# Kernel tuning notes

Hardware: AMD Instinct MI355X
Metric: run time of the kernel (lower is better)

## Reference

```python
import jax, jax.numpy as jnp
import numpy as np

N, M, D = 131072, 8, 128
TAU = 1.0
E_CONST = float(np.e)


def setup_inputs() -> dict:
    key = jax.random.key(0)
    ks = jax.random.split(key, 6)
    x = jax.random.normal(ks[0], (N, M, D), dtype=jnp.float32)
    q = jax.random.uniform(ks[1], (N, M), dtype=jnp.float32)  # per-mode energies
    w = 0.1 * jax.random.uniform(ks[2], (M,), dtype=jnp.float32)
    b = 0.1 * jax.random.uniform(ks[3], (M,), dtype=jnp.float32)
    gammas = jax.random.uniform(ks[4], (M, M), dtype=jnp.float32)  # in (0,1)
    G = 0.1 * jax.random.normal(ks[5], (M,), dtype=jnp.float32)
    bias = jnp.zeros((M,), dtype=jnp.float32)
    qmin = jnp.zeros((M,), dtype=jnp.float32)
    return {"x": x, "q": q, "w": w, "b": b, "gammas": gammas,
            "G": G, "bias": bias, "qmin": qmin}


def reference(x, q, w, b, gammas, G, bias, qmin):
    e = jnp.float32(E_CONST)
    # correction (eval mode): shift by running min, clamp at e so phi > 0
    corr = jnp.maximum(q - qmin[None, :] + e, e)          # [N, M]
    phi = (1.0 + w)[None, :] * corr + b[None, :]          # [N, M]
    # symmetrized gamma: g[i,j] = gammas[min(i,j), max(i,j)]
    idx = jnp.arange(gammas.shape[0])
    g_sym = jnp.where(idx[:, None] < idx[None, :], gammas, gammas.T)  # [M, M]
    # pairwise power-weighted partial energies: phi_i^g * phi_j^(1-g)
    partials = phi[:, :, None] ** g_sym[None] * phi[:, None, :] ** (1.0 - g_sym)[None]  # [N, M, M]
    modal = jnp.sum(partials, axis=-1)                    # [N, M]
    logs = jax.nn.log_softmax(-TAU * modal, axis=-1)
    alphas = jnp.exp(logs)                                # [N, M]
    # gated attention over modes
    betas = jax.nn.relu(jnp.tanh(G[None, :] * alphas + bias[None, :]))  # [N, M]
    return betas[:, :, None] * x                          # [N, M, D]
```

## Files before the change

kernel.cpp:

```cpp
#include <hip/hip_runtime.h>
#include <math.h>

#define NROWS 131072
#define M 8
#define D 128
#define RPB 32
#define E_CONST 2.71828182845904523536f

__global__ __launch_bounds__(256) void emma_fused2(
    const float* __restrict__ x, const float* __restrict__ q,
    const float* __restrict__ w, const float* __restrict__ b,
    const float* __restrict__ gammas, const float* __restrict__ G,
    const float* __restrict__ bias, const float* __restrict__ qmin,
    float* __restrict__ out)
{
    __shared__ float s_beta[RPB][M];

    const int tid = threadIdx.x;
    const int r   = tid >> 3;
    const int i   = tid & 7;
    const int n   = blockIdx.x * RPB + r;

    {
        const float4 q0 = *reinterpret_cast<const float4*>(q + (size_t)n * M);
        const float4 q1 = *reinterpret_cast<const float4*>(q + (size_t)n * M + 4);
        float qv[M] = {q0.x, q0.y, q0.z, q0.w, q1.x, q1.y, q1.z, q1.w};

        float lphi[M];
        #pragma unroll
        for (int m = 0; m < M; ++m) {
            float corr = fmaxf(qv[m] - qmin[m] + E_CONST, E_CONST);
            float phi  = fmaf(w[m], corr, corr) + b[m];
            lphi[m] = logf(phi);
        }

        float myl = lphi[0];
        #pragma unroll
        for (int m = 1; m < M; ++m) if (i == m) myl = lphi[m];

        float s = 0.0f;
        #pragma unroll
        for (int j = 0; j < M; ++j) {
            int lo = (i < j) ? i : j;
            int hi = (i < j) ? j : i;
            float g = gammas[lo * M + hi];
            s += expf(fmaf(g, myl - lphi[j], lphi[j]));
        }

        float neg = -s;
        float mx = neg;
        #pragma unroll
        for (int d = 1; d < 8; d <<= 1) mx = fmaxf(mx, __shfl_xor(mx, d, 8));
        float e = expf(neg - mx);
        float sum = e;
        #pragma unroll
        for (int d = 1; d < 8; d <<= 1) sum += __shfl_xor(sum, d, 8);
        float alpha = e / sum;

        float t = tanhf(fmaf(G[i], alpha, bias[i]));
        s_beta[r][i] = fmaxf(t, 0.0f);
    }
    __syncthreads();

    const size_t base = (size_t)blockIdx.x * (RPB * M * D);
    const float4* __restrict__ x4 = reinterpret_cast<const float4*>(x + base);
    float4* __restrict__ o4       = reinterpret_cast<float4*>(out + base);
    const int mm = tid >> 5;

    #pragma unroll 4
    for (int rr = 0; rr < RPB; ++rr) {
        const float beta = s_beta[rr][mm];
        float4 v = x4[(size_t)rr * 256 + tid];
        v.x *= beta; v.y *= beta; v.z *= beta; v.w *= beta;
        o4[(size_t)rr * 256 + tid] = v;
    }
}

extern "C" void kernel_launch(void* const* d_in, const int* in_sizes, int n_in,
                              void* d_out, int out_size, void* d_ws, size_t ws_size,
                              hipStream_t stream) {
    const float* x      = (const float*)d_in[0];
    const float* q      = (const float*)d_in[1];
    const float* w      = (const float*)d_in[2];
    const float* b      = (const float*)d_in[3];
    const float* gammas = (const float*)d_in[4];
    const float* G      = (const float*)d_in[5];
    const float* bias   = (const float*)d_in[6];
    const float* qmin   = (const float*)d_in[7];
    float* out = (float*)d_out;

    emma_fused2<<<NROWS / RPB, 256, 0, stream>>>(
        x, q, w, b, gammas, G, bias, qmin, out);
}
```

Measured before the change: 214.6 us.

## Skip x loads for zero-gated modes and use nontemporal batched streaming

Reworks the scaling phase so each wave handles units of 32 lanes of float4 for a given row and mode. When every lane in the wave sees beta equal to zero, it writes zeros without reading x at all, which cuts read traffic for modes the ReLU gate turns off. Loads and stores become nontemporal, and eight loads are issued before their stores to keep more memory requests in flight. The skip gives different results if x holds NaN or Inf, where 0*x would not be zero. Its benefit also depends on how many gates are exactly zero.

```diff
diff --git a/kernel.cpp b/kernel.cpp
--- a/kernel.cpp
+++ b/kernel.cpp
@@ -7,7 +7,9 @@
 #define RPB 32
 #define E_CONST 2.71828182845904523536f
 
-__global__ __launch_bounds__(256) void emma_fused2(
+typedef float f32x4 __attribute__((ext_vector_type(4)));
+
+__global__ __launch_bounds__(256) void emma_fused6(
     const float* __restrict__ x, const float* __restrict__ q,
     const float* __restrict__ w, const float* __restrict__ b,
     const float* __restrict__ gammas, const float* __restrict__ G,
@@ -22,8 +24,8 @@
     const int n   = blockIdx.x * RPB + r;
 
     {
-        const float4 q0 = *reinterpret_cast<const float4*>(q + (size_t)n * M);
-        const float4 q1 = *reinterpret_cast<const float4*>(q + (size_t)n * M + 4);
+        const f32x4 q0 = *reinterpret_cast<const f32x4*>(q + (size_t)n * M);
+        const f32x4 q1 = *reinterpret_cast<const f32x4*>(q + (size_t)n * M + 4);
         float qv[M] = {q0.x, q0.y, q0.z, q0.w, q1.x, q1.y, q1.z, q1.w};
 
         float lphi[M];
@@ -62,18 +64,51 @@
     }
     __syncthreads();
 
-    const size_t base = (size_t)blockIdx.x * (RPB * M * D);
-    const float4* __restrict__ x4 = reinterpret_cast<const float4*>(x + base);
-    float4* __restrict__ o4       = reinterpret_cast<float4*>(out + base);
-    const int mm = tid >> 5;
+    const size_t base = (size_t)blockIdx.x * (RPB * M * D / 4);
+    const f32x4* __restrict__ x4 = reinterpret_cast<const f32x4*>(x) + base;
+    f32x4* __restrict__ o4       = reinterpret_cast<f32x4*>(out) + base;
 
-    #pragma unroll 4
-    for (int rr = 0; rr < RPB; ++rr) {
-        const float beta = s_beta[rr][mm];
-        float4 v = x4[(size_t)rr * 256 + tid];
-        v.x *= beta; v.y *= beta; v.z *= beta; v.w *= beta;
-        o4[(size_t)rr * 256 + tid] = v;
+    const int lane = tid & 63;
+    const int wv   = tid >> 6;
+    const int half = lane >> 5;
+    const int l32  = lane & 31;
+    const f32x4 zero4 = {0.f, 0.f, 0.f, 0.f};
+
+#define UNIT(K, UU)                                                          \
+    const int    u##K   = (UU);                                              \
+    const int    row##K = ((u##K >> 3) << 1) + half;                         \
+    const int    md##K  = u##K & 7;                                          \
+    const float  bb##K  = s_beta[row##K][md##K];                             \
+    const size_t a##K   = (size_t)row##K * 256 + md##K * 32 + l32;           \
+    f32x4 v##K;                                                              \
+    if (__all(bb##K == 0.0f)) { v##K = zero4; }                              \
+    else { v##K = __builtin_nontemporal_load(&x4[a##K]); }
+
+#define STOREU(K)                                                            \
+    __builtin_nontemporal_store(v##K * bb##K, &o4[a##K]);
+
+    #pragma unroll
+    for (int g = 0; g < 4; ++g) {
+        UNIT(0, wv + 32 * g +  0)
+        UNIT(1, wv + 32 * g +  4)
+        UNIT(2, wv + 32 * g +  8)
+        UNIT(3, wv + 32 * g + 12)
+        UNIT(4, wv + 32 * g + 16)
+        UNIT(5, wv + 32 * g + 20)
+        UNIT(6, wv + 32 * g + 24)
+        UNIT(7, wv + 32 * g + 28)
+        STOREU(0)
+        STOREU(1)
+        STOREU(2)
+        STOREU(3)
+        STOREU(4)
+        STOREU(5)
+        STOREU(6)
+        STOREU(7)
     }
+
+#undef UNIT
+#undef STOREU
 }
 
 extern "C" void kernel_launch(void* const* d_in, const int* in_sizes, int n_in,
@@ -89,6 +124,6 @@
     const float* qmin   = (const float*)d_in[7];
     float* out = (float*)d_out;
 
-    emma_fused2<<<NROWS / RPB, 256, 0, stream>>>(
+    emma_fused6<<<NROWS / RPB, 256, 0, stream>>>(
         x, q, w, b, gammas, G, bias, qmin, out);
 }
```

Measured after the change: 190.0 us. 1.13x faster.
